# Performance work log

Hardware: AMD Instinct MI355X
Metric: run time of the kernel (lower is better)

Reference implementation:

```python
import jax, jax.numpy as jnp
import numpy as np

B, T, D, H, L = 64, 256, 1024, 1024, 2


def setup_inputs() -> dict:
    key = jax.random.key(0)
    ks = jax.random.split(key, 14)
    s = 1.0 / np.sqrt(H)
    x = jax.random.normal(ks[0], (B, T, D), jnp.float32)
    lengths = jax.random.randint(ks[1], (B,), 1, T + 1)

    def u(k, shape):
        return jax.random.uniform(k, shape, jnp.float32, -s, s)

    # stacked per-layer weights; layer 0 input dim == H so stacking is valid
    fw_Wx = u(ks[2], (L, D, 4 * H))
    fw_Wh = u(ks[3], (L, H, 4 * H))
    fw_b = u(ks[4], (L, 4 * H))  # x2h.bias + h2h.bias folded into one
    bw_Wx = u(ks[5], (L, D, 4 * H))
    bw_Wh = u(ks[6], (L, H, 4 * H))
    bw_b = u(ks[7], (L, 4 * H))
    return dict(x=x, lengths=lengths, fw_Wx=fw_Wx, fw_Wh=fw_Wh, fw_b=fw_b,
                bw_Wx=bw_Wx, bw_Wh=bw_Wh, bw_b=bw_b)


def _run_direction(xs, valid, Wx, Wh, b):
    # xs: [T, B, D] in processing order; valid: [T, B, 1] mask by step index
    n_layers = Wx.shape[0]
    inp = xs
    hT = None
    for l in range(n_layers):
        Wx_l, Wh_l, b_l = Wx[l], Wh[l], b[l]

        def step(carry, sv, Wx_l=Wx_l, Wh_l=Wh_l, b_l=b_l):
            h, c = carry
            x_t, v = sv
            gates = x_t @ Wx_l + h @ Wh_l + b_l  # [B, 4H]
            i, f, g, o = jnp.split(gates, 4, axis=-1)
            c_new = jax.nn.sigmoid(f) * c + jax.nn.sigmoid(i) * jnp.tanh(g)
            h_new = jax.nn.sigmoid(o) * jnp.tanh(c_new)
            h2 = v * h_new + (1.0 - v) * h  # length masking: hold state past length
            c2 = v * c_new + (1.0 - v) * c
            return (h2, c2), h2

        z = jnp.zeros((xs.shape[1], Wh_l.shape[0]), xs.dtype)
        (hT, _), inp = jax.lax.scan(step, (z, z), (inp, valid))
    return inp, hT  # [T, B, H] (processing order), [B, H]


def reference(x, lengths, fw_Wx, fw_Wh, fw_b, bw_Wx, bw_Wh, bw_b):
    xs = jnp.transpose(x, (1, 0, 2))  # [T, B, D]
    # valid[s, b] = lengths[b] > s, indexed by step count (same for both dirs)
    valid = (lengths[None, :] > jnp.arange(T)[:, None]).astype(x.dtype)[:, :, None]
    fw_out, fw_last = _run_direction(xs, valid, fw_Wx, fw_Wh, fw_b)
    bw_out_rev, bw_last = _run_direction(xs[::-1], valid, bw_Wx, bw_Wh, bw_b)
    bw_out = bw_out_rev[::-1]  # back to original time order
    outputs = jnp.transpose(jnp.concatenate([fw_out, bw_out], -1), (1, 0, 2))  # [B, T, 2H]
    final = jnp.concatenate([fw_last, bw_last], -1)  # [B, 2H]
    return outputs, final
```

## Files before the change

kernel.cpp:

```cpp
#include <hip/hip_runtime.h>

#define NB 64
#define NT 256
#define ND 1024
#define NH 1024
#define G4 4096

typedef _Float16 half_t;
typedef half_t v8h __attribute__((ext_vector_type(8)));
typedef half_t h4  __attribute__((ext_vector_type(4)));
typedef float  v4f __attribute__((ext_vector_type(4)));

#define XPLANE ((size_t)NB * NT * ND)
#define HPLANE ((size_t)NB * NH)
#define WREG   16384

__global__ void cvt_x(const float* __restrict__ x, half_t* __restrict__ xh) {
    const int row = blockIdx.x;
    const int b = row >> 8, t = row & 255;
    const int o = threadIdx.x * 4;
    const float4 v = *(const float4*)(x + (size_t)row * ND + o);
    const size_t d = ((size_t)t * NB + b) * ND + o;
    h4 hh;
    hh.x = (half_t)v.x; hh.y = (half_t)v.y;
    hh.z = (half_t)v.z; hh.w = (half_t)v.w;
    *(h4*)(xh + d) = hh;
}

__global__ void transpose_pack(const float* __restrict__ fw_Wx,
                               const float* __restrict__ fw_Wh,
                               const float* __restrict__ bw_Wx,
                               const float* __restrict__ bw_Wh,
                               half_t* __restrict__ WT) {
    const int z = blockIdx.z;
    const int combo = z >> 1;
    const int half  = z & 1;
    const int layer = combo >> 1, dirb = combo & 1;
    const float* src = half ? (dirb ? bw_Wh : fw_Wh) : (dirb ? bw_Wx : fw_Wx);
    src += (size_t)layer * ND * G4;
    const int n0 = blockIdx.x * 64, k0 = blockIdx.y * 64;
    __shared__ float tile[64][65];
    const int t = threadIdx.x;
    #pragma unroll
    for (int it = 0; it < 4; ++it) {
        const int kr = it * 16 + (t >> 4);
        const int nc = (t & 15) * 4;
        const float4 v = *(const float4*)(src + (size_t)(k0 + kr) * G4 + n0 + nc);
        tile[kr][nc + 0] = v.x; tile[kr][nc + 1] = v.y;
        tile[kr][nc + 2] = v.z; tile[kr][nc + 3] = v.w;
    }
    __syncthreads();
    #pragma unroll
    for (int it = 0; it < 4; ++it) {
        const int nr = it * 16 + (t >> 4);
        const int kc = (t & 15) * 4;
        h4 hv;
        hv.x = (half_t)tile[kc + 0][nr];
        hv.y = (half_t)tile[kc + 1][nr];
        hv.z = (half_t)tile[kc + 2][nr];
        hv.w = (half_t)tile[kc + 3][nr];
        const int n = n0 + nr;
        const int kr1 = k0 + kc;
        const int gt = n >> 10, j = n & 1023;
        const int jp = j >> 4, l15j = j & 15;
        const int ki = kr1 >> 5, g2 = (kr1 >> 3) & 3, e0 = kr1 & 7;
        const int lane2 = g2 * 16 + l15j;
        const size_t r = (((size_t)combo * 64 + jp) * 4 + gt) * 2 + half;
        *(h4*)(WT + r * WREG + (size_t)ki * 512 + lane2 * 8 + e0) = hv;
    }
}

__device__ __forceinline__ void store_h2(half_t* p, half_t a, half_t b) {
    union { half_t h[2]; unsigned int u; } v;
    v.h[0] = a; v.h[1] = b;
    __hip_atomic_store((unsigned int*)p, v.u,
                       __ATOMIC_RELAXED, __HIP_MEMORY_SCOPE_AGENT);
}

__global__ __launch_bounds__(512, 2) void lstm_persistent(
        const half_t* __restrict__ xh,
        const int* __restrict__ lengths,
        const float* __restrict__ fw_b, const float* __restrict__ bw_b,
        const half_t* __restrict__ WT,
        half_t* __restrict__ hring,
        float* __restrict__ out,
        int* __restrict__ bar) {
    const int bid = blockIdx.x;
    const int c  = (bid & 7) >> 1;
    const int jp = ((bid >> 3) << 1) | (bid & 1);
    const int layer = c >> 1, dir = c & 1;
    const int tid = threadIdx.x;
    const int wv = tid >> 6, lane = tid & 63;
    const int gt = wv & 3, kh = wv >> 2;
    const int l15 = lane & 15, g = lane >> 4;
    const int j0 = jp * 16;

    const int shf  = tid >> 8;
    const int srow = (tid & 255) >> 2;
    const int sks  = (tid & 3) * 32;
    const int sswz = (srow & 7) << 3;
    const int rswz = (l15 & 7) << 3;

    __shared__ half_t alds[2][2][64][128];
    __shared__ float glds[4][2][NB][17];
    __shared__ float c_lds[NB][17];
    __shared__ float h_lds[NB][17];
    __shared__ float bias_lds[4][16];
    __shared__ int   len_lds[NB];

    for (int e = tid; e < NB * 16; e += 512) {
        c_lds[e >> 4][e & 15] = 0.f;
        h_lds[e >> 4][e & 15] = 0.f;
    }
    if (tid < NB) len_lds[tid] = lengths[tid];
    if (tid < 64) {
        const int gg = tid >> 4, jj = tid & 15;
        const float* bs = dir ? bw_b : fw_b;
        bias_lds[gg][jj] = bs[(size_t)layer * G4 + gg * NH + j0 + jj];
    }

    v8h w[32];
    {
        const half_t* wp = WT + ((((size_t)c * 64 + jp) * 4 + gt) * 2 + kh) * WREG
                         + (size_t)lane * 8;
        #pragma unroll
        for (int ki = 0; ki < 32; ++ki) w[ki] = *(const v8h*)(wp + (size_t)ki * 512);
    }
    #pragma unroll
    for (int ki = 0; ki < 32; ++ki) asm volatile("" : "+a"(w[ki]));
    __syncthreads();

    const int grp = jp >> 4;
    int* gcnt   = bar + (c * 4 + grp) * 16;
    int* root   = bar + 256 + c * 16;
    int* rel    = bar + 512 + c * 16;
    int* relDep = bar + 512 + (c & 1) * 16;

    for (int s = 0; s <= NT; ++s) {
        const bool active = (layer == 0) ? (s < NT) : (s >= 1);
        const int u = (layer == 0) ? s : (s - 1);

        const half_t* bsrc = nullptr;
        if (active) {
            if (shf == 0) {
                if (layer == 0) {
                    const int t = dir ? (NT - 1 - u) : u;
                    bsrc = xh + (size_t)t * NB * ND;
                } else {
                    bsrc = hring + ((size_t)s * 4 + dir) * HPLANE;
                }
            } else {
                bsrc = hring + ((size_t)u * 4 + c) * HPLANE;
            }
        }

        v4f acc[4];
        #pragma unroll
        for (int m = 0; m < 4; ++m) acc[m] = (v4f){0.f, 0.f, 0.f, 0.f};

        v8h sA[4], sB[4];
        if (active) {
            const size_t o0 = (size_t)srow * 1024 + sks;
            #pragma unroll
            for (int i = 0; i < 4; ++i) {
                sA[i] = *(const v8h*)(bsrc + o0 + i * 8);
                sB[i] = *(const v8h*)(bsrc + o0 + 128 + i * 8);
            }
        }

        #pragma unroll
        for (int ci = 0; ci < 8; ++ci) {
            if (active) {
                #pragma unroll
                for (int i = 0; i < 4; ++i)
                    *(v8h*)&alds[ci & 1][shf][srow][(sks + i * 8) ^ sswz]
                        = (ci & 1) ? sB[i] : sA[i];
                if (ci < 6) {
                    const size_t o = (size_t)srow * 1024 + (ci + 2) * 128 + sks;
                    #pragma unroll
                    for (int i = 0; i < 4; ++i) {
                        if (ci & 1) sB[i] = *(const v8h*)(bsrc + o + i * 8);
                        else        sA[i] = *(const v8h*)(bsrc + o + i * 8);
                    }
                }
            }
            __syncthreads();
            if (active) {
                #pragma unroll
                for (int ki = 0; ki < 4; ++ki) {
                    #pragma unroll
                    for (int m = 0; m < 4; ++m) {
                        v8h ah = *(const v8h*)&alds[ci & 1][kh][m * 16 + l15]
                                              [(ki * 32 + g * 8) ^ rswz];
                        acc[m] = __builtin_amdgcn_mfma_f32_16x16x32_f16(
                                     ah, w[ci * 4 + ki], acc[m], 0, 0, 0);
                    }
                }
            }
        }

        if (active) {
            #pragma unroll
            for (int m = 0; m < 4; ++m)
                #pragma unroll
                for (int r = 0; r < 4; ++r)
                    glds[gt][kh][m * 16 + g * 4 + r][l15] = acc[m][r];
        }
        __syncthreads();

        if (active) {
            const int b = tid >> 3, jj0 = (tid & 7) * 2;
            float hpair[2];
            #pragma unroll
            for (int k2 = 0; k2 < 2; ++k2) {
                const int jj = jj0 + k2;
                const float iv = glds[0][0][b][jj] + glds[0][1][b][jj] + bias_lds[0][jj];
                const float fv = glds[1][0][b][jj] + glds[1][1][b][jj] + bias_lds[1][jj];
                const float gv = glds[2][0][b][jj] + glds[2][1][b][jj] + bias_lds[2][jj];
                const float ov = glds[3][0][b][jj] + glds[3][1][b][jj] + bias_lds[3][jj];
                const float cold = c_lds[b][jj];
                const float hold = h_lds[b][jj];
                const float si = 1.f / (1.f + expf(-iv));
                const float sf = 1.f / (1.f + expf(-fv));
                const float so = 1.f / (1.f + expf(-ov));
                const float cn = sf * cold + si * tanhf(gv);
                const float hn = so * tanhf(cn);
                const bool valid = len_lds[b] > u;
                const float c2 = valid ? cn : cold;
                const float h2 = valid ? hn : hold;
                c_lds[b][jj] = c2;
                h_lds[b][jj] = h2;
                hpair[k2] = h2;
                if (layer == 1) {
                    const int tout = dir ? (NT - 1 - u) : u;
                    __builtin_nontemporal_store(
                        h2, &out[((size_t)b * NT + tout) * (2 * NH) + dir * NH + j0 + jj]);
                    if (u == NT - 1)
                        __builtin_nontemporal_store(
                            h2, &out[(size_t)NB * NT * (2 * NH) + (size_t)b * (2 * NH)
                                     + dir * NH + j0 + jj]);
                }
            }
            half_t* hb2 = hring + ((size_t)(u + 1) * 4 + c) * HPLANE
                        + (size_t)b * NH + j0 + jj0;
            store_h2(hb2, (half_t)hpair[0], (half_t)hpair[1]);
        }

        const int phase = s + 1;
        __syncthreads();
        if (tid == 0) {
            const int a = __hip_atomic_fetch_add(gcnt, 1, __ATOMIC_RELAXED,
                                                 __HIP_MEMORY_SCOPE_AGENT) + 1;
            if (a == phase * 16) {
                const int rr = __hip_atomic_fetch_add(root, 1, __ATOMIC_RELAXED,
                                                      __HIP_MEMORY_SCOPE_AGENT) + 1;
                if (rr == phase * 4)
                    __hip_atomic_store(rel, phase, __ATOMIC_RELAXED,
                                       __HIP_MEMORY_SCOPE_AGENT);
            }
            while (__hip_atomic_load(rel, __ATOMIC_RELAXED,
                                     __HIP_MEMORY_SCOPE_AGENT) < phase)
                __builtin_amdgcn_s_sleep(1);
            if (layer == 1) {
                while (__hip_atomic_load(relDep, __ATOMIC_RELAXED,
                                         __HIP_MEMORY_SCOPE_AGENT) < phase)
                    __builtin_amdgcn_s_sleep(1);
            }
        }
        __syncthreads();
    }
}

extern "C" void kernel_launch(void* const* d_in, const int* in_sizes, int n_in,
                              void* d_out, int out_size, void* d_ws, size_t ws_size,
                              hipStream_t stream) {
    (void)in_sizes; (void)n_in; (void)out_size; (void)ws_size;
    const float* x     = (const float*)d_in[0];
    const int*   len   = (const int*)d_in[1];
    const float* fw_Wx = (const float*)d_in[2];
    const float* fw_Wh = (const float*)d_in[3];
    const float* fw_b  = (const float*)d_in[4];
    const float* bw_Wx = (const float*)d_in[5];
    const float* bw_Wh = (const float*)d_in[6];
    const float* bw_b  = (const float*)d_in[7];
    float* out = (float*)d_out;

    char* ws = (char*)d_ws;
    size_t off = 0;
    half_t* WT = (half_t*)(ws + off); off += (size_t)2048 * WREG * 2;
    half_t* xh = (half_t*)(ws + off); off += XPLANE * 2;
    int* bar = (int*)(ws + off); off += 4096;
    half_t* hring = (half_t*)(ws + off);

    hipMemsetAsync(bar, 0, 4096 + (size_t)4 * HPLANE * 2, stream);

    cvt_x<<<NB * NT, 256, 0, stream>>>(x, xh);

    dim3 tg(G4 / 64, ND / 64, 8);
    transpose_pack<<<tg, 256, 0, stream>>>(fw_Wx, fw_Wh, bw_Wx, bw_Wh, WT);

    void* args[] = {(void*)&xh, (void*)&len, (void*)&fw_b, (void*)&bw_b,
                    (void*)&WT, (void*)&hring, (void*)&out, (void*)&bar};
    hipLaunchCooperativeKernel((void*)lstm_persistent, dim3(256), dim3(512),
                               args, 0, stream);
}
```

Baseline: 2.568 ms.

## Split barrier wait so input projection overlaps recurrent-state synchronization

The grid barrier wait moves from the end of each step to the start of the two GEMM halves. The input-side half (x or the previous layer's h) waits only on its dependency, and the recurrent-h half waits on its own chain's release just before it needs it. The input projection can therefore proceed while other blocks are still finishing the previous step. In exchange, the two halves run serially with only half the waves issuing MFMA in each phase, which halves MFMA parallelism per phase and may lengthen the per-step critical path.

```diff
diff --git a/kernel.cpp b/kernel.cpp
--- a/kernel.cpp
+++ b/kernel.cpp
@@ -95,13 +95,12 @@
     const int l15 = lane & 15, g = lane >> 4;
     const int j0 = jp * 16;
 
-    const int shf  = tid >> 8;
-    const int srow = (tid & 255) >> 2;
-    const int sks  = (tid & 3) * 32;
+    const int srow = tid >> 3;
+    const int sseg = (tid & 7) * 32;
     const int sswz = (srow & 7) << 3;
     const int rswz = (l15 & 7) << 3;
 
-    __shared__ half_t alds[2][2][64][128];
+    __shared__ half_t alds[2][64][256];
     __shared__ float glds[4][2][NB][17];
     __shared__ float c_lds[NB][17];
     __shared__ float h_lds[NB][17];
@@ -140,60 +139,95 @@
         const bool active = (layer == 0) ? (s < NT) : (s >= 1);
         const int u = (layer == 0) ? s : (s - 1);
 
-        const half_t* bsrc = nullptr;
-        if (active) {
-            if (shf == 0) {
-                if (layer == 0) {
-                    const int t = dir ? (NT - 1 - u) : u;
-                    bsrc = xh + (size_t)t * NB * ND;
-                } else {
-                    bsrc = hring + ((size_t)s * 4 + dir) * HPLANE;
-                }
-            } else {
-                bsrc = hring + ((size_t)u * 4 + c) * HPLANE;
-            }
-        }
-
         v4f acc[4];
         #pragma unroll
         for (int m = 0; m < 4; ++m) acc[m] = (v4f){0.f, 0.f, 0.f, 0.f};
 
-        v8h sA[4], sB[4];
-        if (active) {
-            const size_t o0 = (size_t)srow * 1024 + sks;
+        if (layer == 1 && tid == 0) {
+            while (__hip_atomic_load(relDep, __ATOMIC_RELAXED,
+                                     __HIP_MEMORY_SCOPE_AGENT) < s)
+                __builtin_amdgcn_s_sleep(1);
+        }
+        __syncthreads();
+
+        const half_t* bsrcA = nullptr;
+        if (active) {
+            if (layer == 0) {
+                const int t = dir ? (NT - 1 - u) : u;
+                bsrcA = xh + (size_t)t * NB * ND;
+            } else {
+                bsrcA = hring + ((size_t)s * 4 + dir) * HPLANE;
+            }
+        }
+
+        v8h sh[4];
+        if (active) {
+            const size_t o0 = (size_t)srow * 1024 + sseg;
             #pragma unroll
-            for (int i = 0; i < 4; ++i) {
-                sA[i] = *(const v8h*)(bsrc + o0 + i * 8);
-                sB[i] = *(const v8h*)(bsrc + o0 + 128 + i * 8);
-            }
-        }
-
+            for (int i = 0; i < 4; ++i) sh[i] = *(const v8h*)(bsrcA + o0 + i * 8);
+        }
         #pragma unroll
-        for (int ci = 0; ci < 8; ++ci) {
+        for (int ci = 0; ci < 4; ++ci) {
             if (active) {
                 #pragma unroll
                 for (int i = 0; i < 4; ++i)
-                    *(v8h*)&alds[ci & 1][shf][srow][(sks + i * 8) ^ sswz]
-                        = (ci & 1) ? sB[i] : sA[i];
-                if (ci < 6) {
-                    const size_t o = (size_t)srow * 1024 + (ci + 2) * 128 + sks;
+                    *(v8h*)&alds[ci & 1][srow][(sseg + i * 8) ^ sswz] = sh[i];
+                if (ci < 3) {
+                    const size_t o = (size_t)srow * 1024 + (ci + 1) * 256 + sseg;
                     #pragma unroll
-                    for (int i = 0; i < 4; ++i) {
-                        if (ci & 1) sB[i] = *(const v8h*)(bsrc + o + i * 8);
-                        else        sA[i] = *(const v8h*)(bsrc + o + i * 8);
-                    }
+                    for (int i = 0; i < 4; ++i) sh[i] = *(const v8h*)(bsrcA + o + i * 8);
                 }
             }
             __syncthreads();
-            if (active) {
-                #pragma unroll
-                for (int ki = 0; ki < 4; ++ki) {
+            if (active && kh == 0) {
+                #pragma unroll
+                for (int ki = 0; ki < 8; ++ki) {
                     #pragma unroll
                     for (int m = 0; m < 4; ++m) {
-                        v8h ah = *(const v8h*)&alds[ci & 1][kh][m * 16 + l15]
+                        v8h ah = *(const v8h*)&alds[ci & 1][m * 16 + l15]
                                               [(ki * 32 + g * 8) ^ rswz];
                         acc[m] = __builtin_amdgcn_mfma_f32_16x16x32_f16(
-                                     ah, w[ci * 4 + ki], acc[m], 0, 0, 0);
+                                     ah, w[ci * 8 + ki], acc[m], 0, 0, 0);
+                    }
+                }
+            }
+        }
+
+        if (tid == 0) {
+            while (__hip_atomic_load(rel, __ATOMIC_RELAXED,
+                                     __HIP_MEMORY_SCOPE_AGENT) < s)
+                __builtin_amdgcn_s_sleep(1);
+        }
+        __syncthreads();
+
+        const half_t* bsrcB = active ? hring + ((size_t)u * 4 + c) * HPLANE : nullptr;
+        if (active) {
+            const size_t o0 = (size_t)srow * 1024 + sseg;
+            #pragma unroll
+            for (int i = 0; i < 4; ++i) sh[i] = *(const v8h*)(bsrcB + o0 + i * 8);
+        }
+        #pragma unroll
+        for (int ci = 0; ci < 4; ++ci) {
+            if (active) {
+                #pragma unroll
+                for (int i = 0; i < 4; ++i)
+                    *(v8h*)&alds[ci & 1][srow][(sseg + i * 8) ^ sswz] = sh[i];
+                if (ci < 3) {
+                    const size_t o = (size_t)srow * 1024 + (ci + 1) * 256 + sseg;
+                    #pragma unroll
+                    for (int i = 0; i < 4; ++i) sh[i] = *(const v8h*)(bsrcB + o + i * 8);
+                }
+            }
+            __syncthreads();
+            if (active && kh == 1) {
+                #pragma unroll
+                for (int ki = 0; ki < 8; ++ki) {
+                    #pragma unroll
+                    for (int m = 0; m < 4; ++m) {
+                        v8h ah = *(const v8h*)&alds[ci & 1][m * 16 + l15]
+                                              [(ki * 32 + g * 8) ^ rswz];
+                        acc[m] = __builtin_amdgcn_mfma_f32_16x16x32_f16(
+                                     ah, w[ci * 8 + ki], acc[m], 0, 0, 0);
                     }
                 }
             }
@@ -246,9 +280,9 @@
             store_h2(hb2, (half_t)hpair[0], (half_t)hpair[1]);
         }
 
-        const int phase = s + 1;
         __syncthreads();
         if (tid == 0) {
+            const int phase = s + 1;
             const int a = __hip_atomic_fetch_add(gcnt, 1, __ATOMIC_RELAXED,
                                                  __HIP_MEMORY_SCOPE_AGENT) + 1;
             if (a == phase * 16) {
@@ -258,16 +292,7 @@
                     __hip_atomic_store(rel, phase, __ATOMIC_RELAXED,
                                        __HIP_MEMORY_SCOPE_AGENT);
             }
-            while (__hip_atomic_load(rel, __ATOMIC_RELAXED,
-                                     __HIP_MEMORY_SCOPE_AGENT) < phase)
-                __builtin_amdgcn_s_sleep(1);
-            if (layer == 1) {
-                while (__hip_atomic_load(relDep, __ATOMIC_RELAXED,
-                                         __HIP_MEMORY_SCOPE_AGENT) < phase)
-                    __builtin_amdgcn_s_sleep(1);
-            }
-        }
-        __syncthreads();
+        }
     }
 }
 
```

Result: slower. 2.801 ms (+9.1%).
